# Optimization experiments

Hardware: AMD Instinct MI355X
Metric: run time of the kernel (lower is better)

The kernel has to match this reference:

```python
import jax, jax.numpy as jnp
import numpy as np
from jax import lax

VOCAB, EMB, H, L_CTX = 5, 64, 256, 100
HG = 2 * H  # generator hidden = 512


def lstm_cell(x, h, c, Wih, Whh, b):
    # PyTorch gate order: i, f, g, o
    z = x @ Wih.T + h @ Whh.T + b
    i, f, g, o = jnp.split(z, 4, axis=-1)
    c = jax.nn.sigmoid(f) * c + jax.nn.sigmoid(i) * jnp.tanh(g)
    h = jax.nn.sigmoid(o) * jnp.tanh(c)
    return h, c


def run_lstm(xs, Wih, Whh, b, hidden):
    # xs: [T, B, D] -> ys: [T, B, hidden]
    B = xs.shape[1]
    h0 = jnp.zeros((B, hidden), xs.dtype)

    def step(carry, x):
        h, c = carry
        h, c = lstm_cell(x, h, c, Wih, Whh, b)
        return (h, c), h

    _, ys = lax.scan(step, (h0, h0), xs)
    return ys


def bidir_layer(xs, Wih, Whh, b):
    # Wih/Whh/b stacked over directions: [2, ...]
    yf = run_lstm(xs, Wih[0], Whh[0], b[0], H)
    yb = run_lstm(xs[::-1], Wih[1], Whh[1], b[1], H)[::-1]
    return jnp.concatenate([yf, yb], axis=-1)  # [T, B, 2H]


def setup_inputs() -> dict:
    key = jax.random.key(0)
    ks = iter(jax.random.split(key, 24))
    s = 1.0 / np.sqrt(H)  # pytorch-style uniform scale -> use normal*s

    def w(shape):
        return (jax.random.normal(next(ks), shape, jnp.float32) * s).astype(jnp.float32)

    B = 1024
    inp = {
        "left_context": jax.random.randint(next(ks), (B, L_CTX), 0, VOCAB),
        "right_context": jax.random.randint(next(ks), (B, L_CTX), 0, VOCAB),
        "target_length": 256,
        "emb": w((VOCAB, EMB)),
        # bidirectional context LSTM, layer 0 (in=64) and layer 1 (in=512)
        "ctx0_Wih": w((2, 4 * H, EMB)),
        "ctx0_Whh": w((2, 4 * H, H)),
        "ctx0_b": w((2, 4 * H)),
        "ctx1_Wih": w((2, 4 * H, 2 * H)),
        "ctx1_Whh": w((2, 4 * H, H)),
        "ctx1_b": w((2, 4 * H)),
        # generator LSTM (hidden=512), layer 0 (in=64) and layer 1 (in=512)
        "gen0_Wih": w((4 * HG, EMB)),
        "gen0_Whh": w((4 * HG, HG)),
        "gen0_b": w((4 * HG,)),
        "gen1_Wih": w((4 * HG, HG)),
        "gen1_Whh": w((4 * HG, HG)),
        "gen1_b": w((4 * HG,)),
        "out_W": w((VOCAB, HG)),
        "out_b": w((VOCAB,)),
    }
    return inp


def reference(left_context, right_context, target_length, emb,
              ctx0_Wih, ctx0_Whh, ctx0_b, ctx1_Wih, ctx1_Whh, ctx1_b,
              gen0_Wih, gen0_Whh, gen0_b, gen1_Wih, gen1_Whh, gen1_b,
              out_W, out_b):
    B = left_context.shape[0]

    def encode(tokens):
        x = emb[tokens].transpose(1, 0, 2)          # [L, B, 64]
        x = bidir_layer(x, ctx0_Wih, ctx0_Whh, ctx0_b)  # dropout: eval -> identity
        x = bidir_layer(x, ctx1_Wih, ctx1_Whh, ctx1_b)
        return x                                     # [L, B, 512]

    left_final = encode(left_context)[-1]            # [B, 512]
    right_final = encode(right_context)[0]           # [B, 512]
    combined = (left_final + right_final) * 0.5

    # h_0 = combined repeated over both generator layers; c_0 = 0
    zeros = jnp.zeros((B, HG), combined.dtype)
    tok0 = jnp.zeros((B,), jnp.int32)

    def dec_step(carry, _):
        h0, c0, h1, c1, tok = carry
        x = emb[tok]                                 # [B, 64]
        h0, c0 = lstm_cell(x, h0, c0, gen0_Wih, gen0_Whh, gen0_b)
        h1, c1 = lstm_cell(h0, h1, c1, gen1_Wih, gen1_Whh, gen1_b)
        logits = h1 @ out_W.T + out_b                # dropout: eval -> identity
        tok = jnp.argmax(logits, axis=-1)
        return (h0, c0, h1, c1, tok), logits

    _, logits = lax.scan(dec_step, (combined, zeros, combined, zeros, tok0),
                         None, length=target_length)
    return logits.transpose(1, 0, 2)                 # [B, T, vocab]
```

## Files before the change

kernel.cpp:

```cpp
#include <hip/hip_runtime.h>


#define L_SEQ 100
#define BATCH 1024
#define HCTX 256
#define HG 512
#define TDEC 256

typedef __attribute__((ext_vector_type(8))) short bf16x8;
typedef __attribute__((ext_vector_type(4))) float f32x4;

__device__ __forceinline__ float sigf(float x){ return 1.0f/(1.0f+expf(-x)); }
__device__ __forceinline__ unsigned short f2bf(float x){
  unsigned int u = __float_as_uint(x);
  return (unsigned short)((u + 0x7fffu + ((u>>16)&1u)) >> 16);
}
__device__ __forceinline__ float bf2f(unsigned short h){
  return __uint_as_float(((unsigned int)h)<<16);
}

__global__ void pack_w(const float* __restrict__ W, int G, int K, int KTtot, int kt0,
                       unsigned short* __restrict__ hi, unsigned short* __restrict__ lo){
  int idx = blockIdx.x*blockDim.x + threadIdx.x;
  int kt_n = K/32;
  int total = (G/16)*kt_n*64;
  if (idx >= total) return;
  int lane = idx & 63;
  int ktl = (idx>>6) % kt_n;
  int gt  = (idx>>6) / kt_n;
  int g = gt*16 + (lane & 15);
  int k = ktl*32 + (lane>>4)*8;
  const float* src = W + (size_t)g*K + k;
  size_t dst = (((size_t)gt*KTtot + (kt0 + ktl))*64 + lane)*8;
  #pragma unroll
  for (int j=0;j<8;j++){
    float x = src[j];
    unsigned short h = f2bf(x);
    hi[dst+j] = h;
    lo[dst+j] = f2bf(x - bf2f(h));
  }
}

__global__ void embprep(const float* __restrict__ emb,
                        const float* __restrict__ c0Wih, const float* __restrict__ c0b,
                        const float* __restrict__ g0Wih, const float* __restrict__ g0b,
                        float* __restrict__ ectx0, float* __restrict__ egen0){
  int idx = blockIdx.x*blockDim.x + threadIdx.x;
  if (idx < 2*5*1024){
    int d = idx / 5120;
    int v = (idx / 1024) % 5;
    int j = idx % 1024;
    const float* w = c0Wih + ((size_t)d*1024 + j)*64;
    const float* e = emb + v*64;
    float s = c0b[d*1024 + j];
    #pragma unroll
    for (int k=0;k<64;k++) s += e[k]*w[k];
    ectx0[idx] = s;
  } else if (idx < 2*5*1024 + 5*2048){
    int i2 = idx - 10240;
    int v = i2 / 2048;
    int j = i2 % 2048;
    const float* w = g0Wih + (size_t)j*64;
    const float* e = emb + v*64;
    float s = g0b[j];
    #pragma unroll
    for (int k=0;k<64;k++) s += e[k]*w[k];
    egen0[i2] = s;
  }
}

__global__ void __launch_bounds__(512,1) ctx_l0_mfma(
    const int* __restrict__ toksL, const int* __restrict__ toksR,
    const float* __restrict__ ectx0,
    const unsigned short* __restrict__ wh, const unsigned short* __restrict__ wl,
    unsigned short* __restrict__ y0Lh, unsigned short* __restrict__ y0Ll,
    unsigned short* __restrict__ y0Rh, unsigned short* __restrict__ y0Rl,
    int force_side)
{
  const int id  = blockIdx.x;
  int dir, side, bx;
  if (force_side < 0){
    dir = (id >> 2) & 1; side = (id >> 3) & 1;
    bx = ((id >> 4) << 2) | (id & 3);
  } else {
    dir = (id >> 2) & 1; side = force_side;
    bx = ((id >> 3) << 2) | (id & 3);
  }
  const int* toks = side ? toksR : toksL;
  unsigned short* y0h = side ? y0Rh : y0Lh;
  unsigned short* y0l = side ? y0Rl : y0Ll;
  const int e0  = bx * 16;
  const int lane = threadIdx.x & 63;
  const int w    = threadIdx.x >> 6;
  const int lo16 = lane & 15, kgrp = lane >> 4;

  __shared__ unsigned short hsh[16*256];
  __shared__ unsigned short hsl[16*256];
  __shared__ float cs[16*256];
  for (int i=threadIdx.x;i<16*256;i+=512){ hsh[i]=0; hsl[i]=0; cs[i]=0.f; }
  __syncthreads();

  const unsigned short* pbh[4][2];
  const unsigned short* pbl[4][2];
  #pragma unroll
  for (int g=0;g<4;g++){
    #pragma unroll
    for (int st=0;st<2;st++){
      int ct = g*16 + w*2 + st;
      size_t off = (size_t)dir*1024*256 + ((size_t)(ct*8)*64 + lane)*8;
      pbh[g][st] = wh + off; pbl[g][st] = wl + off;
    }
  }
  const unsigned aoff0 = (unsigned)(lo16*512 + kgrp*16);
  const unsigned axor  = ((unsigned)(lo16 & 7)) << 4;

  for (int s=0;s<L_SEQ;s++){
    const int t = dir ? (L_SEQ-1-s) : s;
    f32x4 zero = {0.f,0.f,0.f,0.f};
    f32x4 acc[4][2];
    #pragma unroll
    for (int g=0;g<4;g++){
      #pragma unroll
      for (int st=0;st<2;st++) acc[g][st] = zero;
    }
    #pragma unroll 2
    for (int kt=0;kt<8;kt++){
      unsigned ao = (aoff0 + kt*64) ^ axor;
      bf16x8 ah = *(const bf16x8*)((const char*)hsh + ao);
      bf16x8 al = *(const bf16x8*)((const char*)hsl + ao);
      #pragma unroll
      for (int g=0;g<4;g++){
        #pragma unroll
        for (int st=0;st<2;st++){
          bf16x8 bh = *(const bf16x8*)(pbh[g][st] + (size_t)kt*512);
          bf16x8 bl = *(const bf16x8*)(pbl[g][st] + (size_t)kt*512);
          acc[g][st] = __builtin_amdgcn_mfma_f32_16x16x32_bf16(ah,bh,acc[g][st],0,0,0);
          acc[g][st] = __builtin_amdgcn_mfma_f32_16x16x32_bf16(al,bh,acc[g][st],0,0,0);
          acc[g][st] = __builtin_amdgcn_mfma_f32_16x16x32_bf16(ah,bl,acc[g][st],0,0,0);
        }
      }
    }
    __syncthreads();
    int tkr[4];
    #pragma unroll
    for (int r=0;r<4;r++) tkr[r] = toks[(e0 + kgrp*4 + r)*L_SEQ + t];
    #pragma unroll
    for (int st=0;st<2;st++){
      const int unit = w*32 + st*16 + lo16;
      #pragma unroll
      for (int r=0;r<4;r++){
        const int row = kgrp*4 + r;
        const int e = e0 + row;
        const float* ep = ectx0 + ((size_t)(dir*5 + tkr[r]))*1024 + unit;
        float zi = acc[0][st][r] + ep[0];
        float zf = acc[1][st][r] + ep[256];
        float zg = acc[2][st][r] + ep[512];
        float zo = acc[3][st][r] + ep[768];
        int ci = row*256 + unit;
        float c = sigf(zf)*cs[ci] + sigf(zi)*tanhf(zg);
        float h = sigf(zo)*tanhf(c);
        cs[ci] = c;
        unsigned short hb = f2bf(h), lb = f2bf(h - bf2f(hb));
        unsigned hoff = ((unsigned)(row*512 + unit*2)) ^ (((unsigned)(row & 7)) << 4);
        *(unsigned short*)((char*)hsh + hoff) = hb;
        *(unsigned short*)((char*)hsl + hoff) = lb;
        size_t yo = ((size_t)t*BATCH + e)*512 + dir*256 + unit;
        y0h[yo] = hb; y0l[yo] = lb;
      }
    }
    __syncthreads();
  }
}

__global__ void __launch_bounds__(512,1) ctx_l1_mfma(
    const unsigned short* __restrict__ y0Lh, const unsigned short* __restrict__ y0Ll,
    const unsigned short* __restrict__ y0Rh, const unsigned short* __restrict__ y0Rl,
    const unsigned short* __restrict__ wh, const unsigned short* __restrict__ wl,
    const float* __restrict__ bias,
    float* __restrict__ leftF, float* __restrict__ rightF,
    int force_side)
{
  const int id  = blockIdx.x;
  int dir, side, bx;
  if (force_side < 0){
    dir = (id >> 2) & 1; side = (id >> 3) & 1;
    bx = ((id >> 4) << 2) | (id & 3);
  } else {
    dir = (id >> 2) & 1; side = force_side;
    bx = ((id >> 3) << 2) | (id & 3);
  }
  const unsigned short* y0h = side ? y0Rh : y0Lh;
  const unsigned short* y0l = side ? y0Rl : y0Ll;
  float* finals = side ? rightF : leftF;
  const int t_store = side ? 0 : (L_SEQ-1);
  const int e0  = bx * 16;
  const int lane = threadIdx.x & 63;
  const int w    = threadIdx.x >> 6;
  const int lo16 = lane & 15, kgrp = lane >> 4;

  __shared__ unsigned short xsh[16*512];
  __shared__ unsigned short xsl[16*512];
  __shared__ unsigned short hsh[16*256];
  __shared__ unsigned short hsl[16*256];
  __shared__ float cs[16*256];
  for (int i=threadIdx.x;i<16*256;i+=512){ hsh[i]=0; hsl[i]=0; cs[i]=0.f; }

  float bb[4][2];
  #pragma unroll
  for (int g=0;g<4;g++){
    #pragma unroll
    for (int st=0;st<2;st++)
      bb[g][st] = bias[dir*1024 + g*256 + w*32 + st*16 + lo16];
  }
  const unsigned short* pbh[4][2];
  const unsigned short* pbl[4][2];
  #pragma unroll
  for (int g=0;g<4;g++){
    #pragma unroll
    for (int st=0;st<2;st++){
      int ct = g*16 + w*2 + st;
      size_t off = (size_t)dir*1024*768 + ((size_t)(ct*24)*64 + lane)*8;
      pbh[g][st] = wh + off; pbl[g][st] = wl + off;
    }
  }
  const unsigned axor = ((unsigned)(lo16 & 7)) << 4;
  __syncthreads();

  for (int s=0;s<L_SEQ;s++){
    const int t = dir ? (L_SEQ-1-s) : s;
    #pragma unroll
    for (int cc=0; cc<2; cc++){
      int ci = threadIdx.x + cc*512;
      int row = ci >> 6, cr = ci & 63;
      const unsigned short* srcbase = y0h + ((size_t)t*BATCH + e0 + row)*512 + cr*8;
      const unsigned short* srcbasel = y0l + ((size_t)t*BATCH + e0 + row)*512 + cr*8;
      uint4 vh = *(const uint4*)srcbase;
      uint4 vl = *(const uint4*)srcbasel;
      unsigned xo = ((unsigned)(row*1024 + cr*16)) ^ (((unsigned)(row & 7)) << 4);
      *(uint4*)((char*)xsh + xo) = vh;
      *(uint4*)((char*)xsl + xo) = vl;
    }
    __syncthreads();
    f32x4 zero = {0.f,0.f,0.f,0.f};
    f32x4 acc[4][2];
    #pragma unroll
    for (int g=0;g<4;g++){
      #pragma unroll
      for (int st=0;st<2;st++) acc[g][st] = zero;
    }
    #pragma unroll 2
    for (int kt=0;kt<16;kt++){
      unsigned ao = ((unsigned)(lo16*1024 + kt*64 + kgrp*16)) ^ axor;
      bf16x8 ah = *(const bf16x8*)((const char*)xsh + ao);
      bf16x8 al = *(const bf16x8*)((const char*)xsl + ao);
      #pragma unroll
      for (int g=0;g<4;g++){
        #pragma unroll
        for (int st=0;st<2;st++){
          bf16x8 bh = *(const bf16x8*)(pbh[g][st] + (size_t)kt*512);
          bf16x8 bl = *(const bf16x8*)(pbl[g][st] + (size_t)kt*512);
          acc[g][st] = __builtin_amdgcn_mfma_f32_16x16x32_bf16(ah,bh,acc[g][st],0,0,0);
          acc[g][st] = __builtin_amdgcn_mfma_f32_16x16x32_bf16(al,bh,acc[g][st],0,0,0);
          acc[g][st] = __builtin_amdgcn_mfma_f32_16x16x32_bf16(ah,bl,acc[g][st],0,0,0);
        }
      }
    }
    #pragma unroll 2
    for (int kt=16;kt<24;kt++){
      unsigned ao = ((unsigned)(lo16*512 + (kt-16)*64 + kgrp*16)) ^ axor;
      bf16x8 ah = *(const bf16x8*)((const char*)hsh + ao);
      bf16x8 al = *(const bf16x8*)((const char*)hsl + ao);
      #pragma unroll
      for (int g=0;g<4;g++){
        #pragma unroll
        for (int st=0;st<2;st++){
          bf16x8 bh = *(const bf16x8*)(pbh[g][st] + (size_t)kt*512);
          bf16x8 bl = *(const bf16x8*)(pbl[g][st] + (size_t)kt*512);
          acc[g][st] = __builtin_amdgcn_mfma_f32_16x16x32_bf16(ah,bh,acc[g][st],0,0,0);
          acc[g][st] = __builtin_amdgcn_mfma_f32_16x16x32_bf16(al,bh,acc[g][st],0,0,0);
          acc[g][st] = __builtin_amdgcn_mfma_f32_16x16x32_bf16(ah,bl,acc[g][st],0,0,0);
        }
      }
    }
    __syncthreads();
    #pragma unroll
    for (int st=0;st<2;st++){
      const int unit = w*32 + st*16 + lo16;
      #pragma unroll
      for (int r=0;r<4;r++){
        const int row = kgrp*4 + r;
        float zi = acc[0][st][r] + bb[0][st];
        float zf = acc[1][st][r] + bb[1][st];
        float zg = acc[2][st][r] + bb[2][st];
        float zo = acc[3][st][r] + bb[3][st];
        int ci = row*256 + unit;
        float c = sigf(zf)*cs[ci] + sigf(zi)*tanhf(zg);
        float h = sigf(zo)*tanhf(c);
        cs[ci] = c;
        unsigned short hb = f2bf(h), lb = f2bf(h - bf2f(hb));
        unsigned hoff = ((unsigned)(row*512 + unit*2)) ^ (((unsigned)(row & 7)) << 4);
        *(unsigned short*)((char*)hsh + hoff) = hb;
        *(unsigned short*)((char*)hsl + hoff) = lb;
        if (t == t_store)
          finals[(size_t)(e0 + row)*512 + dir*256 + unit] = h;
      }
    }
    __syncthreads();
  }
}

__global__ void combine_init2(const float* __restrict__ lf, const float* __restrict__ rf,
                              unsigned short* __restrict__ h0h, unsigned short* __restrict__ h0l,
                              unsigned short* __restrict__ h1h, unsigned short* __restrict__ h1l,
                              float* __restrict__ c0, float* __restrict__ c1){
  int i = blockIdx.x*blockDim.x + threadIdx.x;
  if (i < BATCH*HG){
    float v = 0.5f*(lf[i]+rf[i]);
    unsigned short h = f2bf(v);
    unsigned short l = f2bf(v - bf2f(h));
    h0h[i]=h; h0l[i]=l; h1h[i]=h; h1l[i]=l;
    c0[i]=0.f; c1[i]=0.f;
  }
}

__global__ void __launch_bounds__(512,1) dec_l0_mfma(
    const float* __restrict__ egen0,
    const unsigned short* __restrict__ wh, const unsigned short* __restrict__ wl,
    const unsigned short* __restrict__ hih, const unsigned short* __restrict__ hil,
    const unsigned short* __restrict__ h1ih, const unsigned short* __restrict__ h1il,
    unsigned short* __restrict__ hoh, unsigned short* __restrict__ hol,
    float* __restrict__ cst,
    const float* __restrict__ outW, const float* __restrict__ outb,
    float* __restrict__ out, int t)
{
  __shared__ unsigned short bsm[2][32768];
  const int bid = blockIdx.x;
  const int by = bid & 15;
  const int bx = bid >> 4;
  const int e0 = bx * 64;
  const int lane = threadIdx.x & 63;
  const int w = threadIdx.x >> 6;
  const int wm = w & 3, wu = w >> 2;
  const int ut = by*2 + wu;
  const int lo16 = lane & 15, kgrp = lane >> 4;
  const int arow = e0 + wm*16 + lo16;
  const int u = ut*16 + lo16;
  const int r0 = e0 + wm*16 + kgrp*4;

  const unsigned short* pah = hih + (size_t)arow*512 + kgrp*8;
  const unsigned short* pal = hil + (size_t)arow*512 + kgrp*8;

  auto STAGE = [&](int c){
    #pragma unroll
    for (int i=0;i<8;i++){
      int id = w*8 + i;
      int hl  = id & 1;
      int q   = (id >> 1) & 3;
      int wu2 = (id >> 3) & 1;
      int ksl = id >> 4;
      int ks  = c*4 + ksl;
      const unsigned short* src = (hl ? wl : wh)
          + (((size_t)(q*32 + by*2 + wu2)*16 + ks)*64 + lane)*8;
      __builtin_amdgcn_global_load_lds((const void*)src,
          (void*)(&bsm[c & 1][id*512]), 16, 0, 0);
    }
  };

  const f32x4 z4 = {0.f,0.f,0.f,0.f};
  f32x4 aHH[4]={z4,z4,z4,z4}, aLH[4]={z4,z4,z4,z4}, aHL[4]={z4,z4,z4,z4};

  STAGE(0);
  __syncthreads();
  for (int c=0; c<4; c++){
    if (c+1 < 4) STAGE(c+1);
    const unsigned short* bb = &bsm[c&1][0];
    #pragma unroll
    for (int ksl=0; ksl<4; ksl++){
      int ks = c*4 + ksl;
      bf16x8 ah = *(const bf16x8*)(pah + (size_t)ks*32);
      bf16x8 al = *(const bf16x8*)(pal + (size_t)ks*32);
      #pragma unroll
      for (int q=0;q<4;q++){
        int fid = ((ksl*2 + wu)*4 + q)*2;
        bf16x8 bh = *(const bf16x8*)(bb + fid*512     + lane*8);
        bf16x8 bl = *(const bf16x8*)(bb + fid*512+512 + lane*8);
        aHH[q] = __builtin_amdgcn_mfma_f32_16x16x32_bf16(ah, bh, aHH[q], 0,0,0);
        aLH[q] = __builtin_amdgcn_mfma_f32_16x16x32_bf16(al, bh, aLH[q], 0,0,0);
        aHL[q] = __builtin_amdgcn_mfma_f32_16x16x32_bf16(ah, bl, aHL[q], 0,0,0);
      }
    }
    __syncthreads();
  }

  int tkr[4] = {0,0,0,0};
  if (t > 0){
    float acc5[4][5];
    #pragma unroll
    for (int r=0;r<4;r++){
      #pragma unroll
      for (int v=0;v<5;v++) acc5[r][v]=0.f;
    }
    #pragma unroll
    for (int j=0;j<4;j++){
      const int ub = lo16*32 + j*8;
      f32x4 w0[5], w1[5];
      #pragma unroll
      for (int v=0;v<5;v++){
        const float* wp = outW + v*512 + ub;
        w0[v] = *(const f32x4*)(wp);
        w1[v] = *(const f32x4*)(wp+4);
      }
      #pragma unroll
      for (int r=0;r<4;r++){
        const unsigned short* hh = h1ih + (size_t)(r0+r)*512 + ub;
        const unsigned short* hl = h1il + (size_t)(r0+r)*512 + ub;
        bf16x8 vh = *(const bf16x8*)hh;
        bf16x8 vl = *(const bf16x8*)hl;
        #pragma unroll
        for (int m=0;m<4;m++){
          float hv = bf2f((unsigned short)vh[m]) + bf2f((unsigned short)vl[m]);
          #pragma unroll
          for (int v=0;v<5;v++) acc5[r][v] += hv * w0[v][m];
        }
        #pragma unroll
        for (int m=0;m<4;m++){
          float hv = bf2f((unsigned short)vh[m+4]) + bf2f((unsigned short)vl[m+4]);
          #pragma unroll
          for (int v=0;v<5;v++) acc5[r][v] += hv * w1[v][m];
        }
      }
    }
    #pragma unroll
    for (int r=0;r<4;r++){
      #pragma unroll
      for (int v=0;v<5;v++){
        float s = acc5[r][v];
        s += __shfl_xor(s, 1);
        s += __shfl_xor(s, 2);
        s += __shfl_xor(s, 4);
        s += __shfl_xor(s, 8);
        acc5[r][v] = s + outb[v];
      }
      float best = acc5[r][0]; int tk = 0;
      if (acc5[r][1] > best){ best = acc5[r][1]; tk = 1; }
      if (acc5[r][2] > best){ best = acc5[r][2]; tk = 2; }
      if (acc5[r][3] > best){ best = acc5[r][3]; tk = 3; }
      if (acc5[r][4] > best){ best = acc5[r][4]; tk = 4; }
      tkr[r] = tk;
    }
    if (by == 0 && wu == 0 && lo16 == 0){
      #pragma unroll
      for (int r=0;r<4;r++){
        float* op = out + ((size_t)(r0+r)*TDEC + (t-1))*5;
        #pragma unroll
        for (int v=0;v<5;v++) op[v] = acc5[r][v];
      }
    }
  }

  #pragma unroll
  for (int r=0;r<4;r++){
    const int e = r0 + r;
    const float* ep = egen0 + (size_t)tkr[r]*2048 + u;
    float zi = aHH[0][r]+aLH[0][r]+aHL[0][r] + ep[0];
    float zf = aHH[1][r]+aLH[1][r]+aHL[1][r] + ep[512];
    float zg = aHH[2][r]+aLH[2][r]+aHL[2][r] + ep[1024];
    float zo = aHH[3][r]+aLH[3][r]+aHL[3][r] + ep[1536];
    const size_t idx = (size_t)e*512 + u;
    float c = sigf(zf)*cst[idx] + sigf(zi)*tanhf(zg);
    float h = sigf(zo)*tanhf(c);
    cst[idx] = c;
    unsigned short hb = f2bf(h);
    hoh[idx] = hb;
    hol[idx] = f2bf(h - bf2f(hb));
  }
}

__global__ void __launch_bounds__(512,1) dec_l1_mfma(
    const unsigned short* __restrict__ xh, const unsigned short* __restrict__ xl,
    const unsigned short* __restrict__ wh, const unsigned short* __restrict__ wl,
    const float* __restrict__ bias,
    const unsigned short* __restrict__ hih, const unsigned short* __restrict__ hil,
    unsigned short* __restrict__ hoh, unsigned short* __restrict__ hol,
    float* __restrict__ cst)
{
  __shared__ unsigned short bsm[2][32768];
  const int bid = blockIdx.x;
  const int by = bid & 15;
  const int bx = bid >> 4;
  const int e0 = bx * 64;
  const int lane = threadIdx.x & 63;
  const int w = threadIdx.x >> 6;
  const int wm = w & 3, wu = w >> 2;
  const int ut = by*2 + wu;
  const int lo16 = lane & 15, kgrp = lane >> 4;
  const int arow = e0 + wm*16 + lo16;
  const int u = ut*16 + lo16;
  const int r0 = e0 + wm*16 + kgrp*4;

  const unsigned short* pxh = xh  + (size_t)arow*512 + kgrp*8;
  const unsigned short* pxl = xl  + (size_t)arow*512 + kgrp*8;
  const unsigned short* pah = hih + (size_t)arow*512 + kgrp*8;
  const unsigned short* pal = hil + (size_t)arow*512 + kgrp*8;

  auto STAGE = [&](int c){
    #pragma unroll
    for (int i=0;i<8;i++){
      int id = w*8 + i;
      int hl  = id & 1;
      int q   = (id >> 1) & 3;
      int wu2 = (id >> 3) & 1;
      int ksl = id >> 4;
      int ks  = c*4 + ksl;
      const unsigned short* src = (hl ? wl : wh)
          + (((size_t)(q*32 + by*2 + wu2)*32 + ks)*64 + lane)*8;
      __builtin_amdgcn_global_load_lds((const void*)src,
          (void*)(&bsm[c & 1][id*512]), 16, 0, 0);
    }
  };

  const f32x4 z4 = {0.f,0.f,0.f,0.f};
  f32x4 aHH[4]={z4,z4,z4,z4}, aLH[4]={z4,z4,z4,z4}, aHL[4]={z4,z4,z4,z4};

  STAGE(0);
  __syncthreads();
  for (int c=0; c<8; c++){
    if (c+1 < 8) STAGE(c+1);
    const unsigned short* bb = &bsm[c&1][0];
    const unsigned short* pAh = (c < 4) ? pxh : pah;
    const unsigned short* pAl = (c < 4) ? pxl : pal;
    const int ksA = (c & 3)*4;
    #pragma unroll
    for (int ksl=0; ksl<4; ksl++){
      bf16x8 ah = *(const bf16x8*)(pAh + (size_t)(ksA+ksl)*32);
      bf16x8 al = *(const bf16x8*)(pAl + (size_t)(ksA+ksl)*32);
      #pragma unroll
      for (int q=0;q<4;q++){
        int fid = ((ksl*2 + wu)*4 + q)*2;
        bf16x8 bh = *(const bf16x8*)(bb + fid*512     + lane*8);
        bf16x8 bl = *(const bf16x8*)(bb + fid*512+512 + lane*8);
        aHH[q] = __builtin_amdgcn_mfma_f32_16x16x32_bf16(ah, bh, aHH[q], 0,0,0);
        aLH[q] = __builtin_amdgcn_mfma_f32_16x16x32_bf16(al, bh, aLH[q], 0,0,0);
        aHL[q] = __builtin_amdgcn_mfma_f32_16x16x32_bf16(ah, bl, aHL[q], 0,0,0);
      }
    }
    __syncthreads();
  }

  const float b0 = bias[u], b1 = bias[512+u], b2 = bias[1024+u], b3 = bias[1536+u];
  #pragma unroll
  for (int r=0;r<4;r++){
    const int e = r0 + r;
    float zi = aHH[0][r]+aLH[0][r]+aHL[0][r] + b0;
    float zf = aHH[1][r]+aLH[1][r]+aHL[1][r] + b1;
    float zg = aHH[2][r]+aLH[2][r]+aHL[2][r] + b2;
    float zo = aHH[3][r]+aLH[3][r]+aHL[3][r] + b3;
    const size_t idx = (size_t)e*512 + u;
    float c = sigf(zf)*cst[idx] + sigf(zi)*tanhf(zg);
    float h = sigf(zo)*tanhf(c);
    cst[idx] = c;
    unsigned short hb = f2bf(h);
    hoh[idx] = hb;
    hol[idx] = f2bf(h - bf2f(hb));
  }
}

__global__ void dec_outF(const unsigned short* __restrict__ h1h,
                         const unsigned short* __restrict__ h1l,
                         const float* __restrict__ outW,
                         const float* __restrict__ outb,
                         float* __restrict__ out){
  const int lane = threadIdx.x & 63;
  const int e = blockIdx.x*4 + (threadIdx.x >> 6);
  const unsigned short* hh = h1h + (size_t)e*512;
  const unsigned short* hl = h1l + (size_t)e*512;
  float s0=0,s1=0,s2=0,s3=0,s4=0;
  for (int k=lane;k<512;k+=64){
    float hv = bf2f(hh[k]) + bf2f(hl[k]);
    s0 += hv*outW[k];
    s1 += hv*outW[512+k];
    s2 += hv*outW[1024+k];
    s3 += hv*outW[1536+k];
    s4 += hv*outW[2048+k];
  }
  #pragma unroll
  for (int off=32; off>0; off>>=1){
    s0 += __shfl_down(s0, off);
    s1 += __shfl_down(s1, off);
    s2 += __shfl_down(s2, off);
    s3 += __shfl_down(s3, off);
    s4 += __shfl_down(s4, off);
  }
  if (lane==0){
    float* op = out + ((size_t)e*TDEC + (TDEC-1))*5;
    op[0]=s0+outb[0]; op[1]=s1+outb[1]; op[2]=s2+outb[2];
    op[3]=s3+outb[3]; op[4]=s4+outb[4];
  }
}

extern "C" void kernel_launch(void* const* d_in, const int* in_sizes, int n_in,
                              void* d_out, int out_size, void* d_ws, size_t ws_size,
                              hipStream_t stream){
  (void)in_sizes; (void)n_in; (void)out_size;
  const int*   leftc    = (const int*)d_in[0];
  const int*   rightc   = (const int*)d_in[1];
  const float* emb      = (const float*)d_in[3];
  const float* ctx0_Wih = (const float*)d_in[4];
  const float* ctx0_Whh = (const float*)d_in[5];
  const float* ctx0_b   = (const float*)d_in[6];
  const float* ctx1_Wih = (const float*)d_in[7];
  const float* ctx1_Whh = (const float*)d_in[8];
  const float* ctx1_b   = (const float*)d_in[9];
  const float* gen0_Wih = (const float*)d_in[10];
  const float* gen0_Whh = (const float*)d_in[11];
  const float* gen0_b   = (const float*)d_in[12];
  const float* gen1_Wih = (const float*)d_in[13];
  const float* gen1_Whh = (const float*)d_in[14];
  const float* gen1_b   = (const float*)d_in[15];
  const float* out_W    = (const float*)d_in[16];
  const float* out_b    = (const float*)d_in[17];
  float* out = (float*)d_out;

  char* p = (char*)d_ws;
  auto carve = [&](size_t nfloats)->float*{
    float* r = (float*)p;
    p += ((nfloats*sizeof(float) + 255) & ~(size_t)255);
    return r;
  };
  auto carveu = [&](size_t nush)->unsigned short*{
    return (unsigned short*)carve((nush + 1)/2);
  };
  float* ectx0  = carve(2*5*1024);
  float* egen0  = carve(5*2048);
  float* leftF  = carve((size_t)BATCH*HG);
  float* rightF = carve((size_t)BATCH*HG);
  float* c0s    = carve((size_t)BATCH*HG);
  float* c1s    = carve((size_t)BATCH*HG);
  unsigned short* c0pkh = carveu((size_t)2*1024*256);
  unsigned short* c0pkl = carveu((size_t)2*1024*256);
  unsigned short* c1pkh = carveu((size_t)2*1024*768);
  unsigned short* c1pkl = carveu((size_t)2*1024*768);
  unsigned short* pk0h = carveu((size_t)2048*512);
  unsigned short* pk0l = carveu((size_t)2048*512);
  unsigned short* pk1h = carveu((size_t)2048*1024);
  unsigned short* pk1l = carveu((size_t)2048*1024);
  unsigned short* h0ha = carveu((size_t)BATCH*HG);
  unsigned short* h0la = carveu((size_t)BATCH*HG);
  unsigned short* h0hb = carveu((size_t)BATCH*HG);
  unsigned short* h0lb = carveu((size_t)BATCH*HG);
  unsigned short* h1ha = carveu((size_t)BATCH*HG);
  unsigned short* h1la = carveu((size_t)BATCH*HG);
  unsigned short* h1hb = carveu((size_t)BATCH*HG);
  unsigned short* h1lb = carveu((size_t)BATCH*HG);
  const size_t y0n = (size_t)L_SEQ*BATCH*512;
  unsigned short* y0Lh = carveu(y0n);
  unsigned short* y0Ll = carveu(y0n);
  if ((size_t)(p - (char*)d_ws) > ws_size) return;

  unsigned short* y0Rh = nullptr;
  unsigned short* y0Rl = nullptr;
  {
    size_t used = (size_t)(p - (char*)d_ws);
    size_t need = 2 * (((y0n*sizeof(unsigned short) + 255) & ~(size_t)255));
    if (used + need <= ws_size){
      y0Rh = carveu(y0n);
      y0Rl = carveu(y0n);
    }
  }
  const bool merged = (y0Rh != nullptr);

  for (int d=0; d<2; d++){
    pack_w<<<128, 256, 0, stream>>>(ctx0_Whh + (size_t)d*1024*256, 1024, 256, 8, 0,
                                    c0pkh + (size_t)d*262144, c0pkl + (size_t)d*262144);
    pack_w<<<256, 256, 0, stream>>>(ctx1_Wih + (size_t)d*1024*512, 1024, 512, 24, 0,
                                    c1pkh + (size_t)d*786432, c1pkl + (size_t)d*786432);
    pack_w<<<128, 256, 0, stream>>>(ctx1_Whh + (size_t)d*1024*256, 1024, 256, 24, 16,
                                    c1pkh + (size_t)d*786432, c1pkl + (size_t)d*786432);
  }
  pack_w<<<512, 256, 0, stream>>>(gen0_Whh, 2048, 512, 16,  0, pk0h, pk0l);
  pack_w<<<512, 256, 0, stream>>>(gen1_Wih, 2048, 512, 32,  0, pk1h, pk1l);
  pack_w<<<512, 256, 0, stream>>>(gen1_Whh, 2048, 512, 32, 16, pk1h, pk1l);

  embprep<<<(20480+255)/256, 256, 0, stream>>>(emb, ctx0_Wih, ctx0_b,
                                               gen0_Wih, gen0_b, ectx0, egen0);

  if (merged){
    ctx_l0_mfma<<<256, 512, 0, stream>>>(leftc, rightc, ectx0, c0pkh, c0pkl,
                                         y0Lh, y0Ll, y0Rh, y0Rl, -1);
    ctx_l1_mfma<<<256, 512, 0, stream>>>(y0Lh, y0Ll, y0Rh, y0Rl,
                                         c1pkh, c1pkl, ctx1_b, leftF, rightF, -1);
  } else {
    ctx_l0_mfma<<<128, 512, 0, stream>>>(leftc, rightc, ectx0, c0pkh, c0pkl,
                                         y0Lh, y0Ll, y0Lh, y0Ll, 0);
    ctx_l1_mfma<<<128, 512, 0, stream>>>(y0Lh, y0Ll, y0Lh, y0Ll,
                                         c1pkh, c1pkl, ctx1_b, leftF, rightF, 0);
    ctx_l0_mfma<<<128, 512, 0, stream>>>(leftc, rightc, ectx0, c0pkh, c0pkl,
                                         y0Lh, y0Ll, y0Lh, y0Ll, 1);
    ctx_l1_mfma<<<128, 512, 0, stream>>>(y0Lh, y0Ll, y0Lh, y0Ll,
                                         c1pkh, c1pkl, ctx1_b, leftF, rightF, 1);
  }

  combine_init2<<<(BATCH*HG+255)/256, 256, 0, stream>>>(leftF, rightF,
                                                        h0ha, h0la, h1ha, h1la,
                                                        c0s, c1s);

  for (int t=0;t<TDEC;t++){
    unsigned short* h0ih = (t&1)? h0hb : h0ha;
    unsigned short* h0il = (t&1)? h0lb : h0la;
    unsigned short* h0oh = (t&1)? h0ha : h0hb;
    unsigned short* h0ol = (t&1)? h0la : h0lb;
    unsigned short* h1ih = (t&1)? h1hb : h1ha;
    unsigned short* h1il = (t&1)? h1lb : h1la;
    unsigned short* h1oh = (t&1)? h1ha : h1hb;
    unsigned short* h1ol = (t&1)? h1la : h1lb;
    dec_l0_mfma<<<256, 512, 0, stream>>>(egen0, pk0h, pk0l,
                                         h0ih, h0il, h1ih, h1il,
                                         h0oh, h0ol, c0s,
                                         out_W, out_b, out, t);
    dec_l1_mfma<<<256, 512, 0, stream>>>(h0oh, h0ol, pk1h, pk1l, gen1_b,
                                         h1ih, h1il, h1oh, h1ol, c1s);
  }
  dec_outF<<<256, 256, 0, stream>>>(h1ha, h1la, out_W, out_b, out);
}
```

Baseline: 22.95 ms.

## Fuse decoder layers into one step kernel with precomputed next-step layer-0 gates

Merges the two per-timestep decoder kernels into a single dec_step kernel, halving launches per step. Layer-0's recurrent matmul for the next step is computed at the end of the current step and written as pre-activations (z0), so the next step only adds the token embedding term before the cell update. Each block recomputes the full 64x512 layer-0 hidden tile redundantly into LDS (across 16 by-blocks) so layer-1 and the next layer-0 matmul can read it locally. Weights are now read directly from global memory instead of staged through LDS, and the fp32 z0 buffers add extra global traffic.

```diff
diff --git a/kernel.cpp b/kernel.cpp
--- a/kernel.cpp
+++ b/kernel.cpp
@@ -309,31 +309,25 @@
   }
 }
 
-__global__ void combine_init2(const float* __restrict__ lf, const float* __restrict__ rf,
+__global__ void combine_init3(const float* __restrict__ lf, const float* __restrict__ rf,
                               unsigned short* __restrict__ h0h, unsigned short* __restrict__ h0l,
                               unsigned short* __restrict__ h1h, unsigned short* __restrict__ h1l,
-                              float* __restrict__ c0, float* __restrict__ c1){
+                              float* __restrict__ c0a, float* __restrict__ c1){
   int i = blockIdx.x*blockDim.x + threadIdx.x;
   if (i < BATCH*HG){
     float v = 0.5f*(lf[i]+rf[i]);
     unsigned short h = f2bf(v);
     unsigned short l = f2bf(v - bf2f(h));
     h0h[i]=h; h0l[i]=l; h1h[i]=h; h1l[i]=l;
-    c0[i]=0.f; c1[i]=0.f;
-  }
-}
-
-__global__ void __launch_bounds__(512,1) dec_l0_mfma(
-    const float* __restrict__ egen0,
+    c0a[i]=0.f; c1[i]=0.f;
+  }
+}
+
+__global__ void __launch_bounds__(512,1) z0prep(
+    const unsigned short* __restrict__ h0h, const unsigned short* __restrict__ h0l,
     const unsigned short* __restrict__ wh, const unsigned short* __restrict__ wl,
-    const unsigned short* __restrict__ hih, const unsigned short* __restrict__ hil,
-    const unsigned short* __restrict__ h1ih, const unsigned short* __restrict__ h1il,
-    unsigned short* __restrict__ hoh, unsigned short* __restrict__ hol,
-    float* __restrict__ cst,
-    const float* __restrict__ outW, const float* __restrict__ outb,
-    float* __restrict__ out, int t)
+    float* __restrict__ z0)
 {
-  __shared__ unsigned short bsm[2][32768];
   const int bid = blockIdx.x;
   const int by = bid & 15;
   const int bx = bid >> 4;
@@ -347,50 +341,64 @@
   const int u = ut*16 + lo16;
   const int r0 = e0 + wm*16 + kgrp*4;
 
-  const unsigned short* pah = hih + (size_t)arow*512 + kgrp*8;
-  const unsigned short* pal = hil + (size_t)arow*512 + kgrp*8;
-
-  auto STAGE = [&](int c){
-    #pragma unroll
-    for (int i=0;i<8;i++){
-      int id = w*8 + i;
-      int hl  = id & 1;
-      int q   = (id >> 1) & 3;
-      int wu2 = (id >> 3) & 1;
-      int ksl = id >> 4;
-      int ks  = c*4 + ksl;
-      const unsigned short* src = (hl ? wl : wh)
-          + (((size_t)(q*32 + by*2 + wu2)*16 + ks)*64 + lane)*8;
-      __builtin_amdgcn_global_load_lds((const void*)src,
-          (void*)(&bsm[c & 1][id*512]), 16, 0, 0);
-    }
-  };
-
+  const unsigned short* pah = h0h + (size_t)arow*512 + kgrp*8;
+  const unsigned short* pal = h0l + (size_t)arow*512 + kgrp*8;
+  const unsigned short* pb[8];
+  #pragma unroll
+  for (int q=0;q<4;q++){
+    size_t off = ((size_t)(q*32+ut)*16*64 + lane)*8;
+    pb[q]   = wh + off;
+    pb[q+4] = wl + off;
+  }
   const f32x4 z4 = {0.f,0.f,0.f,0.f};
   f32x4 aHH[4]={z4,z4,z4,z4}, aLH[4]={z4,z4,z4,z4}, aHL[4]={z4,z4,z4,z4};
-
-  STAGE(0);
-  __syncthreads();
-  for (int c=0; c<4; c++){
-    if (c+1 < 4) STAGE(c+1);
-    const unsigned short* bb = &bsm[c&1][0];
-    #pragma unroll
-    for (int ksl=0; ksl<4; ksl++){
-      int ks = c*4 + ksl;
-      bf16x8 ah = *(const bf16x8*)(pah + (size_t)ks*32);
-      bf16x8 al = *(const bf16x8*)(pal + (size_t)ks*32);
-      #pragma unroll
-      for (int q=0;q<4;q++){
-        int fid = ((ksl*2 + wu)*4 + q)*2;
-        bf16x8 bh = *(const bf16x8*)(bb + fid*512     + lane*8);
-        bf16x8 bl = *(const bf16x8*)(bb + fid*512+512 + lane*8);
-        aHH[q] = __builtin_amdgcn_mfma_f32_16x16x32_bf16(ah, bh, aHH[q], 0,0,0);
-        aLH[q] = __builtin_amdgcn_mfma_f32_16x16x32_bf16(al, bh, aLH[q], 0,0,0);
-        aHL[q] = __builtin_amdgcn_mfma_f32_16x16x32_bf16(ah, bl, aHL[q], 0,0,0);
-      }
-    }
-    __syncthreads();
-  }
+  #pragma unroll 2
+  for (int ks=0; ks<16; ks++){
+    bf16x8 ah = *(const bf16x8*)(pah + (size_t)ks*32);
+    bf16x8 al = *(const bf16x8*)(pal + (size_t)ks*32);
+    #pragma unroll
+    for (int q=0;q<4;q++){
+      bf16x8 bh = *(const bf16x8*)(pb[q]   + (size_t)ks*512);
+      bf16x8 bl = *(const bf16x8*)(pb[q+4] + (size_t)ks*512);
+      aHH[q] = __builtin_amdgcn_mfma_f32_16x16x32_bf16(ah, bh, aHH[q], 0,0,0);
+      aLH[q] = __builtin_amdgcn_mfma_f32_16x16x32_bf16(al, bh, aLH[q], 0,0,0);
+      aHL[q] = __builtin_amdgcn_mfma_f32_16x16x32_bf16(ah, bl, aHL[q], 0,0,0);
+    }
+  }
+  #pragma unroll
+  for (int r=0;r<4;r++){
+    #pragma unroll
+    for (int q=0;q<4;q++)
+      z0[(size_t)(r0+r)*2048 + q*512 + u] = aHH[q][r]+aLH[q][r]+aHL[q][r];
+  }
+}
+
+__global__ void __launch_bounds__(512,1) dec_step(
+    const float* __restrict__ egen0,
+    const unsigned short* __restrict__ w0h, const unsigned short* __restrict__ w0l,
+    const unsigned short* __restrict__ w1h, const unsigned short* __restrict__ w1l,
+    const float* __restrict__ bias1,
+    const float* __restrict__ outW, const float* __restrict__ outb,
+    const float* __restrict__ z0cur, float* __restrict__ z0nxt,
+    const float* __restrict__ c0cur, float* __restrict__ c0nxt,
+    const unsigned short* __restrict__ h1ih, const unsigned short* __restrict__ h1il,
+    unsigned short* __restrict__ h1oh, unsigned short* __restrict__ h1ol,
+    float* __restrict__ c1s,
+    float* __restrict__ out, int t)
+{
+  __shared__ unsigned short hsh[64*512];
+  __shared__ unsigned short hsl[64*512];
+  const int bid = blockIdx.x;
+  const int by = bid & 15;
+  const int bx = bid >> 4;
+  const int e0 = bx * 64;
+  const int lane = threadIdx.x & 63;
+  const int w = threadIdx.x >> 6;
+  const int wm = w & 3, wu = w >> 2;
+  const int ut = by*2 + wu;
+  const int lo16 = lane & 15, kgrp = lane >> 4;
+  const int u = ut*16 + lo16;
+  const int r0 = e0 + wm*16 + kgrp*4;
 
   int tkr[4] = {0,0,0,0};
   if (t > 0){
@@ -458,110 +466,139 @@
     }
   }
 
-  #pragma unroll
-  for (int r=0;r<4;r++){
-    const int e = r0 + r;
-    const float* ep = egen0 + (size_t)tkr[r]*2048 + u;
-    float zi = aHH[0][r]+aLH[0][r]+aHL[0][r] + ep[0];
-    float zf = aHH[1][r]+aLH[1][r]+aHL[1][r] + ep[512];
-    float zg = aHH[2][r]+aLH[2][r]+aHL[2][r] + ep[1024];
-    float zo = aHH[3][r]+aLH[3][r]+aHL[3][r] + ep[1536];
-    const size_t idx = (size_t)e*512 + u;
-    float c = sigf(zf)*cst[idx] + sigf(zi)*tanhf(zg);
-    float h = sigf(zo)*tanhf(c);
-    cst[idx] = c;
-    unsigned short hb = f2bf(h);
-    hoh[idx] = hb;
-    hol[idx] = f2bf(h - bf2f(hb));
-  }
-}
-
-__global__ void __launch_bounds__(512,1) dec_l1_mfma(
-    const unsigned short* __restrict__ xh, const unsigned short* __restrict__ xl,
-    const unsigned short* __restrict__ wh, const unsigned short* __restrict__ wl,
-    const float* __restrict__ bias,
-    const unsigned short* __restrict__ hih, const unsigned short* __restrict__ hil,
-    unsigned short* __restrict__ hoh, unsigned short* __restrict__ hol,
-    float* __restrict__ cst)
-{
-  __shared__ unsigned short bsm[2][32768];
-  const int bid = blockIdx.x;
-  const int by = bid & 15;
-  const int bx = bid >> 4;
-  const int e0 = bx * 64;
-  const int lane = threadIdx.x & 63;
-  const int w = threadIdx.x >> 6;
-  const int wm = w & 3, wu = w >> 2;
-  const int ut = by*2 + wu;
-  const int lo16 = lane & 15, kgrp = lane >> 4;
-  const int arow = e0 + wm*16 + lo16;
-  const int u = ut*16 + lo16;
-  const int r0 = e0 + wm*16 + kgrp*4;
-
-  const unsigned short* pxh = xh  + (size_t)arow*512 + kgrp*8;
-  const unsigned short* pxl = xl  + (size_t)arow*512 + kgrp*8;
-  const unsigned short* pah = hih + (size_t)arow*512 + kgrp*8;
-  const unsigned short* pal = hil + (size_t)arow*512 + kgrp*8;
-
-  auto STAGE = [&](int c){
-    #pragma unroll
-    for (int i=0;i<8;i++){
-      int id = w*8 + i;
-      int hl  = id & 1;
-      int q   = (id >> 1) & 3;
-      int wu2 = (id >> 3) & 1;
-      int ksl = id >> 4;
-      int ks  = c*4 + ksl;
-      const unsigned short* src = (hl ? wl : wh)
-          + (((size_t)(q*32 + by*2 + wu2)*32 + ks)*64 + lane)*8;
-      __builtin_amdgcn_global_load_lds((const void*)src,
-          (void*)(&bsm[c & 1][id*512]), 16, 0, 0);
-    }
-  };
-
-  const f32x4 z4 = {0.f,0.f,0.f,0.f};
-  f32x4 aHH[4]={z4,z4,z4,z4}, aLH[4]={z4,z4,z4,z4}, aHL[4]={z4,z4,z4,z4};
-
-  STAGE(0);
+  {
+    const int ub = (wu*16 + lo16)*16;
+    #pragma unroll
+    for (int r=0;r<4;r++){
+      const int grow = r0 + r;
+      const int lr = wm*16 + kgrp*4 + r;
+      const float* zp = z0cur + (size_t)grow*2048 + ub;
+      const float* ep = egen0 + (size_t)tkr[r]*2048 + ub;
+      const float* cp = c0cur + (size_t)grow*512 + ub;
+      float* cn = c0nxt + (size_t)grow*512 + ub;
+      unsigned short hbuf[16], lbuf[16];
+      #pragma unroll
+      for (int jc=0;jc<4;jc++){
+        f32x4 zvi = *(const f32x4*)(zp + jc*4);
+        f32x4 zvf = *(const f32x4*)(zp + 512 + jc*4);
+        f32x4 zvg = *(const f32x4*)(zp + 1024 + jc*4);
+        f32x4 zvo = *(const f32x4*)(zp + 1536 + jc*4);
+        f32x4 evi = *(const f32x4*)(ep + jc*4);
+        f32x4 evf = *(const f32x4*)(ep + 512 + jc*4);
+        f32x4 evg = *(const f32x4*)(ep + 1024 + jc*4);
+        f32x4 evo = *(const f32x4*)(ep + 1536 + jc*4);
+        f32x4 c0v = *(const f32x4*)(cp + jc*4);
+        #pragma unroll
+        for (int m=0;m<4;m++){
+          float c = sigf(zvf[m]+evf[m])*c0v[m] + sigf(zvi[m]+evi[m])*tanhf(zvg[m]+evg[m]);
+          float h = sigf(zvo[m]+evo[m])*tanhf(c);
+          if (by == 0) cn[jc*4+m] = c;
+          unsigned short hb = f2bf(h);
+          hbuf[jc*4+m] = hb;
+          lbuf[jc*4+m] = f2bf(h - bf2f(hb));
+        }
+      }
+      #pragma unroll
+      for (int k2=0;k2<2;k2++){
+        unsigned ad = ((unsigned)(lr*1024 + ub*2 + k2*16)) ^ (((unsigned)(lr & 7)) << 4);
+        *(uint4*)((char*)hsh + ad) = *(const uint4*)(&hbuf[k2*8]);
+        *(uint4*)((char*)hsl + ad) = *(const uint4*)(&lbuf[k2*8]);
+      }
+    }
+  }
   __syncthreads();
-  for (int c=0; c<8; c++){
-    if (c+1 < 8) STAGE(c+1);
-    const unsigned short* bb = &bsm[c&1][0];
-    const unsigned short* pAh = (c < 4) ? pxh : pah;
-    const unsigned short* pAl = (c < 4) ? pxl : pal;
-    const int ksA = (c & 3)*4;
-    #pragma unroll
-    for (int ksl=0; ksl<4; ksl++){
-      bf16x8 ah = *(const bf16x8*)(pAh + (size_t)(ksA+ksl)*32);
-      bf16x8 al = *(const bf16x8*)(pAl + (size_t)(ksA+ksl)*32);
+
+  const int lr2 = wm*16 + lo16;
+  const unsigned axor2 = ((unsigned)(lr2 & 7)) << 4;
+
+  {
+    const unsigned short* pah = h1ih + (size_t)(e0 + lr2)*512 + kgrp*8;
+    const unsigned short* pal = h1il + (size_t)(e0 + lr2)*512 + kgrp*8;
+    const unsigned short* pb[8];
+    #pragma unroll
+    for (int q=0;q<4;q++){
+      size_t off = ((size_t)(q*32+ut)*32*64 + lane)*8;
+      pb[q]   = w1h + off;
+      pb[q+4] = w1l + off;
+    }
+    const f32x4 z4 = {0.f,0.f,0.f,0.f};
+    f32x4 aHH[4]={z4,z4,z4,z4}, aLH[4]={z4,z4,z4,z4}, aHL[4]={z4,z4,z4,z4};
+    #pragma unroll 2
+    for (int ks=0; ks<16; ks++){
+      unsigned ao = ((unsigned)(lr2*1024 + (ks*32 + kgrp*8)*2)) ^ axor2;
+      bf16x8 ah = *(const bf16x8*)((const char*)hsh + ao);
+      bf16x8 al = *(const bf16x8*)((const char*)hsl + ao);
       #pragma unroll
       for (int q=0;q<4;q++){
-        int fid = ((ksl*2 + wu)*4 + q)*2;
-        bf16x8 bh = *(const bf16x8*)(bb + fid*512     + lane*8);
-        bf16x8 bl = *(const bf16x8*)(bb + fid*512+512 + lane*8);
+        bf16x8 bh = *(const bf16x8*)(pb[q]   + (size_t)ks*512);
+        bf16x8 bl = *(const bf16x8*)(pb[q+4] + (size_t)ks*512);
         aHH[q] = __builtin_amdgcn_mfma_f32_16x16x32_bf16(ah, bh, aHH[q], 0,0,0);
         aLH[q] = __builtin_amdgcn_mfma_f32_16x16x32_bf16(al, bh, aLH[q], 0,0,0);
         aHL[q] = __builtin_amdgcn_mfma_f32_16x16x32_bf16(ah, bl, aHL[q], 0,0,0);
       }
     }
-    __syncthreads();
-  }
-
-  const float b0 = bias[u], b1 = bias[512+u], b2 = bias[1024+u], b3 = bias[1536+u];
-  #pragma unroll
-  for (int r=0;r<4;r++){
-    const int e = r0 + r;
-    float zi = aHH[0][r]+aLH[0][r]+aHL[0][r] + b0;
-    float zf = aHH[1][r]+aLH[1][r]+aHL[1][r] + b1;
-    float zg = aHH[2][r]+aLH[2][r]+aHL[2][r] + b2;
-    float zo = aHH[3][r]+aLH[3][r]+aHL[3][r] + b3;
-    const size_t idx = (size_t)e*512 + u;
-    float c = sigf(zf)*cst[idx] + sigf(zi)*tanhf(zg);
-    float h = sigf(zo)*tanhf(c);
-    cst[idx] = c;
-    unsigned short hb = f2bf(h);
-    hoh[idx] = hb;
-    hol[idx] = f2bf(h - bf2f(hb));
+    #pragma unroll 2
+    for (int ks=16; ks<32; ks++){
+      bf16x8 ah = *(const bf16x8*)(pah + (size_t)(ks-16)*32);
+      bf16x8 al = *(const bf16x8*)(pal + (size_t)(ks-16)*32);
+      #pragma unroll
+      for (int q=0;q<4;q++){
+        bf16x8 bh = *(const bf16x8*)(pb[q]   + (size_t)ks*512);
+        bf16x8 bl = *(const bf16x8*)(pb[q+4] + (size_t)ks*512);
+        aHH[q] = __builtin_amdgcn_mfma_f32_16x16x32_bf16(ah, bh, aHH[q], 0,0,0);
+        aLH[q] = __builtin_amdgcn_mfma_f32_16x16x32_bf16(al, bh, aLH[q], 0,0,0);
+        aHL[q] = __builtin_amdgcn_mfma_f32_16x16x32_bf16(ah, bl, aHL[q], 0,0,0);
+      }
+    }
+    const float b0 = bias1[u], b1 = bias1[512+u];
+    const float b2 = bias1[1024+u], b3 = bias1[1536+u];
+    #pragma unroll
+    for (int r=0;r<4;r++){
+      const int e = r0 + r;
+      float zi = aHH[0][r]+aLH[0][r]+aHL[0][r] + b0;
+      float zf = aHH[1][r]+aLH[1][r]+aHL[1][r] + b1;
+      float zg = aHH[2][r]+aLH[2][r]+aHL[2][r] + b2;
+      float zo = aHH[3][r]+aLH[3][r]+aHL[3][r] + b3;
+      const size_t idx = (size_t)e*512 + u;
+      float c = sigf(zf)*c1s[idx] + sigf(zi)*tanhf(zg);
+      float h = sigf(zo)*tanhf(c);
+      c1s[idx] = c;
+      unsigned short hb = f2bf(h);
+      h1oh[idx] = hb;
+      h1ol[idx] = f2bf(h - bf2f(hb));
+    }
+  }
+
+  if (t < TDEC-1){
+    const unsigned short* pb[8];
+    #pragma unroll
+    for (int q=0;q<4;q++){
+      size_t off = ((size_t)(q*32+ut)*16*64 + lane)*8;
+      pb[q]   = w0h + off;
+      pb[q+4] = w0l + off;
+    }
+    const f32x4 z4 = {0.f,0.f,0.f,0.f};
+    f32x4 aHH[4]={z4,z4,z4,z4}, aLH[4]={z4,z4,z4,z4}, aHL[4]={z4,z4,z4,z4};
+    #pragma unroll 2
+    for (int ks=0; ks<16; ks++){
+      unsigned ao = ((unsigned)(lr2*1024 + (ks*32 + kgrp*8)*2)) ^ axor2;
+      bf16x8 ah = *(const bf16x8*)((const char*)hsh + ao);
+      bf16x8 al = *(const bf16x8*)((const char*)hsl + ao);
+      #pragma unroll
+      for (int q=0;q<4;q++){
+        bf16x8 bh = *(const bf16x8*)(pb[q]   + (size_t)ks*512);
+        bf16x8 bl = *(const bf16x8*)(pb[q+4] + (size_t)ks*512);
+        aHH[q] = __builtin_amdgcn_mfma_f32_16x16x32_bf16(ah, bh, aHH[q], 0,0,0);
+        aLH[q] = __builtin_amdgcn_mfma_f32_16x16x32_bf16(al, bh, aLH[q], 0,0,0);
+        aHL[q] = __builtin_amdgcn_mfma_f32_16x16x32_bf16(ah, bl, aHL[q], 0,0,0);
+      }
+    }
+    #pragma unroll
+    for (int r=0;r<4;r++){
+      #pragma unroll
+      for (int q=0;q<4;q++)
+        z0nxt[(size_t)(r0+r)*2048 + q*512 + u] = aHH[q][r]+aLH[q][r]+aHL[q][r];
+    }
   }
 }
 
@@ -634,8 +671,11 @@
   float* egen0  = carve(5*2048);
   float* leftF  = carve((size_t)BATCH*HG);
   float* rightF = carve((size_t)BATCH*HG);
-  float* c0s    = carve((size_t)BATCH*HG);
+  float* c0a    = carve((size_t)BATCH*HG);
+  float* c0b    = carve((size_t)BATCH*HG);
   float* c1s    = carve((size_t)BATCH*HG);
+  float* z0a    = carve((size_t)BATCH*4*HG);
+  float* z0b    = carve((size_t)BATCH*4*HG);
   unsigned short* c0pkh = carveu((size_t)2*1024*256);
   unsigned short* c0pkl = carveu((size_t)2*1024*256);
   unsigned short* c1pkh = carveu((size_t)2*1024*768);
@@ -646,8 +686,6 @@
   unsigned short* pk1l = carveu((size_t)2048*1024);
   unsigned short* h0ha = carveu((size_t)BATCH*HG);
   unsigned short* h0la = carveu((size_t)BATCH*HG);
-  unsigned short* h0hb = carveu((size_t)BATCH*HG);
-  unsigned short* h0lb = carveu((size_t)BATCH*HG);
   unsigned short* h1ha = carveu((size_t)BATCH*HG);
   unsigned short* h1la = carveu((size_t)BATCH*HG);
   unsigned short* h1hb = carveu((size_t)BATCH*HG);
@@ -700,25 +738,25 @@
                                          c1pkh, c1pkl, ctx1_b, leftF, rightF, 1);
   }
 
-  combine_init2<<<(BATCH*HG+255)/256, 256, 0, stream>>>(leftF, rightF,
+  combine_init3<<<(BATCH*HG+255)/256, 256, 0, stream>>>(leftF, rightF,
                                                         h0ha, h0la, h1ha, h1la,
-                                                        c0s, c1s);
+                                                        c0a, c1s);
+  z0prep<<<256, 512, 0, stream>>>(h0ha, h0la, pk0h, pk0l, z0a);
 
   for (int t=0;t<TDEC;t++){
-    unsigned short* h0ih = (t&1)? h0hb : h0ha;
-    unsigned short* h0il = (t&1)? h0lb : h0la;
-    unsigned short* h0oh = (t&1)? h0ha : h0hb;
-    unsigned short* h0ol = (t&1)? h0la : h0lb;
+    const float* z0cur = (t&1)? z0b : z0a;
+    float*       z0nxt = (t&1)? z0a : z0b;
+    const float* c0cur = (t&1)? c0b : c0a;
+    float*       c0nxt = (t&1)? c0a : c0b;
     unsigned short* h1ih = (t&1)? h1hb : h1ha;
     unsigned short* h1il = (t&1)? h1lb : h1la;
     unsigned short* h1oh = (t&1)? h1ha : h1hb;
     unsigned short* h1ol = (t&1)? h1la : h1lb;
-    dec_l0_mfma<<<256, 512, 0, stream>>>(egen0, pk0h, pk0l,
-                                         h0ih, h0il, h1ih, h1il,
-                                         h0oh, h0ol, c0s,
-                                         out_W, out_b, out, t);
-    dec_l1_mfma<<<256, 512, 0, stream>>>(h0oh, h0ol, pk1h, pk1l, gen1_b,
-                                         h1ih, h1il, h1oh, h1ol, c1s);
+    dec_step<<<256, 512, 0, stream>>>(egen0, pk0h, pk0l, pk1h, pk1l, gen1_b,
+                                      out_W, out_b,
+                                      z0cur, z0nxt, c0cur, c0nxt,
+                                      h1ih, h1il, h1oh, h1ol, c1s,
+                                      out, t);
   }
   dec_outF<<<256, 256, 0, stream>>>(h1ha, h1la, out_W, out_b, out);
 }
```

Result: slower. 35.63 ms (+55.3%).
